# Optimization experiments

Hardware: AMD Instinct MI355X
Metric: run time of the kernel (lower is better)

The kernel has to match this reference:

```python
import jax, jax.numpy as jnp
import numpy as np

B = 20000       # batch (labeled) nodes
N1 = 80000      # first-order neighbor nodes
E = 800000      # edges in the sampled subgraph over B+N1 nodes
C_IN = 256
C_OUT = 256
NUM_D = 32
NB = C_IN // NUM_D   # 8 branches
NUM_M = 4096
NUM_N = 200000  # total graph nodes (c_indices buffer length)


def setup_inputs() -> dict:
    key = jax.random.key(0)
    ks = jax.random.split(key, 12)
    x = jax.random.normal(ks[0], (B, C_IN), dtype=jnp.float32)
    edge_index = jax.random.randint(ks[1], (2, E), 0, B + N1, dtype=jnp.int32)
    edge_weight = jax.random.uniform(ks[2], (E,), dtype=jnp.float32)
    c_indices = jax.random.randint(ks[3], (NB, NUM_N), 0, NUM_M, dtype=jnp.int32)
    first_order_idx = jax.random.randint(ks[4], (N1,), 0, NUM_N, dtype=jnp.int32)
    codebook = jax.random.normal(ks[5], (NB, NUM_M, 2 * NUM_D), dtype=jnp.float32)
    s = 1.0 / np.sqrt(C_IN)
    W_conv = jax.random.normal(ks[6], (C_IN, C_IN), dtype=jnp.float32) * s
    b_conv = jnp.zeros((C_IN,), dtype=jnp.float32)
    W_t = jax.random.normal(ks[7], (C_IN, C_OUT), dtype=jnp.float32) * s
    b_t = jnp.zeros((C_OUT,), dtype=jnp.float32)
    W_skip = jax.random.normal(ks[8], (C_IN, C_OUT), dtype=jnp.float32) * s
    b_skip = jnp.zeros((C_OUT,), dtype=jnp.float32)
    warm_up_rate = jnp.ones((1,), dtype=jnp.float32)
    return {
        'x': x, 'edge_weight': edge_weight, 'codebook': codebook,
        'W_conv': W_conv, 'b_conv': b_conv, 'W_t': W_t, 'b_t': b_t,
        'W_skip': W_skip, 'b_skip': b_skip, 'warm_up_rate': warm_up_rate,
        'c_indices': c_indices, 'first_order_idx': first_order_idx,
        'edge_index': edge_index,
    }


def reference(x, edge_weight, codebook, W_conv, b_conv, W_t, b_t,
              W_skip, b_skip, warm_up_rate, c_indices, first_order_idx,
              edge_index):
    nb = codebook.shape[0]
    D = codebook.shape[2] // 2
    n_total = x.shape[0] + first_order_idx.shape[0]

    # per-branch VQ codebook gather for first-order neighbors: [nb, N1, 2D]
    c_idx = c_indices[:, first_order_idx]                       # [nb, N1]
    cb = codebook[jnp.arange(nb)[:, None], c_idx]               # [nb, N1, 2D]
    # concat branches along feature dim -> [N1, nb*D]
    x_first_order = cb[:, :, :D].transpose(1, 0, 2).reshape(-1, nb * D)
    grad_first_order = cb[:, :, D:].transpose(1, 0, 2).reshape(-1, nb * D)

    # x_input = [batch rows; quantized neighbor rows]
    x_input = jnp.concatenate([x, x_first_order], axis=0)       # [B+N1, C]

    # GCN conv (normalize=False): aggregate (x@W) over weighted edges + bias
    xw = x_input @ W_conv                                       # [B+N1, C]
    msg = xw[edge_index[0]] * edge_weight[:, None]              # [E, C]
    x_output = jax.ops.segment_sum(msg, edge_index[1],
                                   num_segments=n_total) + b_conv

    # info_backward term (gradient pathway through quantized neighbors)
    info_backward = jnp.sum(x_output[x.shape[0]:] * grad_first_order) \
        * warm_up_rate[0]

    # output transform + skip connection on batch rows only
    out = x_output[:x.shape[0]] @ W_t + b_t + (x @ W_skip + b_skip)
    return out, info_backward
```

## Files before the change

### kernel.cpp

```cpp
#include <hip/hip_runtime.h>

#define B_NODES 20000
#define N1_NODES 80000
#define NTOT 100000
#define E_EDGES 800000
#define CIN 256
#define COUT 256
#define NUM_D 32
#define NB 8
#define NUM_M 4096
#define NUM_N 200000
#define NPART 2048
#define CAP 40
#define NXCVT 313
#define NZERO 100
#define NG1 3126
#define EPB 256
#define NG2 626

typedef __attribute__((ext_vector_type(8))) short short8;
typedef __attribute__((ext_vector_type(8))) unsigned short ushort8;
typedef __attribute__((ext_vector_type(4))) float f32x4;
typedef __attribute__((ext_vector_type(4))) int i32x4;

__device__ inline unsigned short f2bf(float f) {
    unsigned int u = __float_as_uint(f);
    u += 0x7FFFu + ((u >> 16) & 1u);
    return (unsigned short)(u >> 16);
}
__device__ inline float bf2f(unsigned short u) {
    return __uint_as_float((unsigned int)u << 16);
}

__device__ inline short8 pack2(float4 a, float4 b) {
    short8 r;
    r[0] = (short)f2bf(a.x); r[1] = (short)f2bf(a.y);
    r[2] = (short)f2bf(a.z); r[3] = (short)f2bf(a.w);
    r[4] = (short)f2bf(b.x); r[5] = (short)f2bf(b.y);
    r[6] = (short)f2bf(b.z); r[7] = (short)f2bf(b.w);
    return r;
}

__global__ __launch_bounds__(256) void prepw_kernel(
    const float* __restrict__ Wc, const float* __restrict__ Wt,
    const float* __restrict__ Ws, short* __restrict__ WcT,
    short* __restrict__ WoT, const float* __restrict__ x,
    unsigned short* __restrict__ xb, int* __restrict__ cnt)
{
    __shared__ float Ls[64][65];
    if (blockIdx.x < 48) {
        const int z   = blockIdx.x >> 4;
        const int rem = blockIdx.x & 15;
        const int kx  = rem & 3, ny = rem >> 2;
        const float* src = (z == 0) ? Wc : ((z == 1) ? Wt : Ws);
        short* dst = (z == 0) ? WcT : WoT;
        const int dstStride = (z == 0) ? 256 : 512;
        const int colOff = (z == 2) ? 256 : 0;

        const int k0 = kx * 64, n0 = ny * 64;
        const int tid = threadIdx.x;
        #pragma unroll
        for (int lp = 0; lp < 16; ++lp) {
            int idx = tid + lp * 256;
            int rr = idx >> 6, cc = idx & 63;
            Ls[rr][cc] = src[(size_t)(k0 + rr) * 256 + n0 + cc];
        }
        __syncthreads();
        #pragma unroll
        for (int lp = 0; lp < 16; ++lp) {
            int idx = tid + lp * 256;
            int rr = idx >> 6, cc = idx & 63;
            dst[(size_t)(n0 + rr) * dstStride + colOff + k0 + cc] =
                (short)f2bf(Ls[cc][rr]);
        }
    } else if (blockIdx.x < 48 + NXCVT) {
        const int base = (blockIdx.x - 48) * 256 + threadIdx.x;
        const int total8 = B_NODES * CIN / 8;
        for (int g = base; g < total8; g += NXCVT * 256) {
            const float4* src = (const float4*)(x + (size_t)g * 8);
            *(short8*)(xb + (size_t)g * 8) = pack2(src[0], src[1]);
        }
    } else {
        const int base = (blockIdx.x - 48 - NXCVT) * 256 + threadIdx.x;
        const int total4 = (NTOT + NPART) / 4;
        i32x4 z = {0, 0, 0, 0};
        for (int g = base; g < total4; g += NZERO * 256)
            ((i32x4*)cnt)[g] = z;
    }
}

__global__ __launch_bounds__(256) void gemm1_scat_kernel(
    const unsigned short* __restrict__ xb, const int* __restrict__ fo,
    const int* __restrict__ cind, const float* __restrict__ cb,
    const short* __restrict__ WcT, unsigned short* __restrict__ xwb,
    const int* __restrict__ ei, const float* __restrict__ ew,
    int* __restrict__ cnt, int2* __restrict__ esw)
{
    __shared__ short As[2][64 * 40];
    __shared__ short Bs[2][128 * 40];

    const int tid  = threadIdx.x;
    const int w    = tid >> 6, l = tid & 63;
    const int row0 = (blockIdx.x >> 1) * 64;
    const int colbase = (blockIdx.x & 1) * 128;
    const int r    = tid >> 2, q = tid & 3;
    const int bc_  = tid >> 1, bq = tid & 1;
    const int grow = row0 + r;
    const int g16  = (l >> 4) * 8;

    f32x4 acc[4][2] = {};

    for (int kso = 0; kso < 4; ++kso) {
        #pragma unroll
        for (int h = 0; h < 2; ++h) {
            const int ks = kso * 2 + h;
            const int k0 = ks * 32;
            short8 sv = {0,0,0,0,0,0,0,0};
            if (grow < B_NODES) {
                sv = *(const short8*)(xb + (size_t)grow * CIN + k0 + q * 8);
            } else if (grow < NTOT) {
                int i = grow - B_NODES;
                int cidx = cind[ks * NUM_N + fo[i]];
                const float4* src = (const float4*)(cb +
                    ((size_t)(ks * NUM_M + cidx)) * (2 * NUM_D) + q * 8);
                sv = pack2(src[0], src[1]);
            }
            *(short8*)&As[h][r * 40 + q * 8] = sv;

            const short8* wp = (const short8*)(WcT +
                (size_t)(colbase + bc_) * 256 + k0 + bq * 16);
            short8* bd = (short8*)&Bs[h][bc_ * 40 + bq * 16];
            bd[0] = wp[0]; bd[1] = wp[1];
        }
        __syncthreads();

        #pragma unroll
        for (int h = 0; h < 2; ++h) {
            short8 av[4], bv[2];
            #pragma unroll
            for (int m = 0; m < 4; ++m)
                av[m] = *(const short8*)&As[h][((l & 15) + 16 * m) * 40 + g16];
            #pragma unroll
            for (int n = 0; n < 2; ++n)
                bv[n] = *(const short8*)&Bs[h][((l & 15) + 16 * n + w * 32) * 40 + g16];
            #pragma unroll
            for (int m = 0; m < 4; ++m)
                #pragma unroll
                for (int n = 0; n < 2; ++n)
                    acc[m][n] = __builtin_amdgcn_mfma_f32_16x16x32_bf16(
                        av[m], bv[n], acc[m][n], 0, 0, 0);
        }
        __syncthreads();
    }

    #pragma unroll
    for (int m = 0; m < 4; ++m) {
        int rbase = row0 + 16 * m + (l >> 4) * 4;
        #pragma unroll
        for (int n = 0; n < 2; ++n) {
            int col = colbase + w * 32 + 16 * n + (l & 15);
            #pragma unroll
            for (int j = 0; j < 4; ++j) {
                int rr = rbase + j;
                if (rr < NTOT)
                    xwb[(size_t)rr * COUT + col] = f2bf(acc[m][n][j]);
            }
        }
    }

    int e = blockIdx.x * EPB + tid;
    if (e < E_EDGES) {
        int dst = ei[E_EDGES + e];
        int pos = atomicAdd(&cnt[dst], 1);
        esw[(size_t)dst * CAP + pos] = make_int2(ei[e], __float_as_int(ew[e]));
    }
}

__global__ __launch_bounds__(256) void gather_accum_kernel(
    const unsigned short* __restrict__ xwb, const int2* __restrict__ esw,
    const int* __restrict__ cnt, const float* __restrict__ b_conv,
    const int* __restrict__ fo, const int* __restrict__ cind,
    const float* __restrict__ cb,
    unsigned short* __restrict__ xoutb, float* __restrict__ scalpart)
{
    const int wid  = threadIdx.x >> 6;
    const int lane = threadIdx.x & 63;
    const int node = blockIdx.x * 4 + wid;
    if (node >= NTOT) return;

    const int half = lane >> 5;
    const int l32  = lane & 31;
    const int c0   = l32 * 8;

    float acc[8];
    if (half == 0) {
        float4 b0 = *(const float4*)(b_conv + c0);
        float4 b1 = *(const float4*)(b_conv + c0 + 4);
        acc[0] = b0.x; acc[1] = b0.y; acc[2] = b0.z; acc[3] = b0.w;
        acc[4] = b1.x; acc[5] = b1.y; acc[6] = b1.z; acc[7] = b1.w;
    } else {
        #pragma unroll
        for (int k = 0; k < 8; ++k) acc[k] = 0.0f;
    }

    const int s = node * CAP;
    const int e = s + cnt[node];
    for (int j = s; j < e; j += 8) {
        int2  p[4];
        float w[4];
        #pragma unroll
        for (int t = 0; t < 4; ++t) {
            int idx = j + 2 * t + half;
            bool valid = idx < e;
            p[t] = esw[valid ? idx : s];
            w[t] = valid ? __int_as_float(p[t].y) : 0.0f;
        }
        ushort8 u[4];
        #pragma unroll
        for (int t = 0; t < 4; ++t)
            u[t] = *(const ushort8*)(xwb + (size_t)p[t].x * CIN + c0);
        #pragma unroll
        for (int t = 0; t < 4; ++t) {
            #pragma unroll
            for (int k = 0; k < 8; ++k) acc[k] += bf2f(u[t][k]) * w[t];
        }
    }

    #pragma unroll
    for (int k = 0; k < 8; ++k) acc[k] += __shfl_xor(acc[k], 32, 64);

    if (node < B_NODES) {
        if (half == 0) {
            ushort8 o;
            #pragma unroll
            for (int k = 0; k < 8; ++k) o[k] = f2bf(acc[k]);
            *(ushort8*)(xoutb + (size_t)node * CIN + c0) = o;
        }
    } else {
        float v = 0.0f;
        if (half == 0) {
            int i = node - B_NODES;
            int b = l32 >> 2;
            int d = (l32 & 3) * 8;
            int cidx = cind[b * NUM_N + fo[i]];
            const float* gp = cb + ((size_t)(b * NUM_M + cidx)) * (2 * NUM_D)
                              + NUM_D + d;
            float4 g0 = *(const float4*)gp;
            float4 g1 = *(const float4*)(gp + 4);
            v = acc[0] * g0.x + acc[1] * g0.y + acc[2] * g0.z + acc[3] * g0.w
              + acc[4] * g1.x + acc[5] * g1.y + acc[6] * g1.z + acc[7] * g1.w;
        }
        #pragma unroll
        for (int off = 32; off > 0; off >>= 1) v += __shfl_down(v, off, 64);
        if (lane == 0)
            atomicAdd(&scalpart[node & (NPART - 1)], v);
    }
}

__global__ __launch_bounds__(256) void gemm2_fin_kernel(
    const unsigned short* __restrict__ xoutb, const unsigned short* __restrict__ xb,
    const short* __restrict__ WoT,
    const float* __restrict__ bt, const float* __restrict__ bskip,
    const float* __restrict__ scalpart, const float* __restrict__ wur,
    float* __restrict__ out)
{
    if (blockIdx.x == NG2) {
        __shared__ float wsum[4];
        float v = 0.0f;
        for (int i = threadIdx.x; i < NPART; i += 256) v += scalpart[i];
        #pragma unroll
        for (int off = 32; off > 0; off >>= 1) v += __shfl_down(v, off, 64);
        if ((threadIdx.x & 63) == 0) wsum[threadIdx.x >> 6] = v;
        __syncthreads();
        if (threadIdx.x == 0)
            out[(size_t)B_NODES * COUT] =
                (wsum[0] + wsum[1] + wsum[2] + wsum[3]) * wur[0];
        return;
    }

    __shared__ short As[2][64 * 40];
    __shared__ short Bs[2][128 * 40];
    __shared__ float bsum[128];

    const int tid  = threadIdx.x;
    const int w    = tid >> 6, l = tid & 63;
    const int row0 = (blockIdx.x >> 1) * 64;
    const int colbase = (blockIdx.x & 1) * 128;
    const int r    = tid >> 2, q = tid & 3;
    const int bc_  = tid >> 1, bq = tid & 1;
    const int grow = row0 + r;
    const int g16  = (l >> 4) * 8;

    if (tid < 128) bsum[tid] = bt[colbase + tid] + bskip[colbase + tid];

    f32x4 acc[4][2] = {};

    for (int kso = 0; kso < 8; ++kso) {
        #pragma unroll
        for (int h = 0; h < 2; ++h) {
            const int ks = kso * 2 + h;
            const int k0 = ks * 32;
            short8 sv = {0,0,0,0,0,0,0,0};
            if (grow < B_NODES) {
                const unsigned short* base = (ks < 8)
                    ? (xoutb + (size_t)grow * CIN + k0)
                    : (xb    + (size_t)grow * CIN + (k0 - 256));
                sv = *(const short8*)(base + q * 8);
            }
            *(short8*)&As[h][r * 40 + q * 8] = sv;

            const short8* wp = (const short8*)(WoT +
                (size_t)(colbase + bc_) * 512 + k0 + bq * 16);
            short8* bd = (short8*)&Bs[h][bc_ * 40 + bq * 16];
            bd[0] = wp[0]; bd[1] = wp[1];
        }
        __syncthreads();

        #pragma unroll
        for (int h = 0; h < 2; ++h) {
            short8 av[4], bv[2];
            #pragma unroll
            for (int m = 0; m < 4; ++m)
                av[m] = *(const short8*)&As[h][((l & 15) + 16 * m) * 40 + g16];
            #pragma unroll
            for (int n = 0; n < 2; ++n)
                bv[n] = *(const short8*)&Bs[h][((l & 15) + 16 * n + w * 32) * 40 + g16];
            #pragma unroll
            for (int m = 0; m < 4; ++m)
                #pragma unroll
                for (int n = 0; n < 2; ++n)
                    acc[m][n] = __builtin_amdgcn_mfma_f32_16x16x32_bf16(
                        av[m], bv[n], acc[m][n], 0, 0, 0);
        }
        __syncthreads();
    }

    #pragma unroll
    for (int m = 0; m < 4; ++m) {
        int rbase = row0 + 16 * m + (l >> 4) * 4;
        #pragma unroll
        for (int n = 0; n < 2; ++n) {
            int lcol = w * 32 + 16 * n + (l & 15);
            int col  = colbase + lcol;
            float bc = bsum[lcol];
            #pragma unroll
            for (int j = 0; j < 4; ++j) {
                int rr = rbase + j;
                if (rr < B_NODES)
                    out[(size_t)rr * COUT + col] = acc[m][n][j] + bc;
            }
        }
    }
}

extern "C" void kernel_launch(void* const* d_in, const int* in_sizes, int n_in,
                              void* d_out, int out_size, void* d_ws, size_t ws_size,
                              hipStream_t stream)
{
    const float* x       = (const float*)d_in[0];
    const float* ew      = (const float*)d_in[1];
    const float* cb      = (const float*)d_in[2];
    const float* W_conv  = (const float*)d_in[3];
    const float* b_conv  = (const float*)d_in[4];
    const float* W_t     = (const float*)d_in[5];
    const float* b_t     = (const float*)d_in[6];
    const float* W_skip  = (const float*)d_in[7];
    const float* b_skip  = (const float*)d_in[8];
    const float* wur     = (const float*)d_in[9];
    const int*   cind    = (const int*)d_in[10];
    const int*   fo      = (const int*)d_in[11];
    const int*   ei      = (const int*)d_in[12];

    float* out = (float*)d_out;

    unsigned short* xwb   = (unsigned short*)d_ws;
    unsigned short* xoutb = xwb + (size_t)NTOT * CIN;
    unsigned short* xb    = xoutb + (size_t)B_NODES * CIN;
    short* WcT      = (short*)(xb + (size_t)B_NODES * CIN);
    short* WoT      = WcT + 256 * 256;
    int2*  esw      = (int2*)(WoT + 256 * 512);
    int*   cnt      = (int*)(esw + (size_t)NTOT * CAP);
    float* scalpart = (float*)(cnt + NTOT);

    prepw_kernel<<<48 + NXCVT + NZERO, 256, 0, stream>>>(
        W_conv, W_t, W_skip, WcT, WoT, x, xb, cnt);

    gemm1_scat_kernel<<<NG1, 256, 0, stream>>>(
        xb, fo, cind, cb, WcT, xwb, ei, ew, cnt, esw);

    gather_accum_kernel<<<NTOT / 4, 256, 0, stream>>>(
        xwb, esw, cnt, b_conv, fo, cind, cb, xoutb, scalpart);

    gemm2_fin_kernel<<<NG2 + 1, 256, 0, stream>>>(
        xoutb, xb, WoT, b_t, b_skip, scalpart, wur, out);
}
```

Before: 178.0 us.

## Widen GEMM1 tiles to full 256 columns with 512-thread blocks

The first GEMM now uses 512-thread blocks that each compute a 64x256 output tile, instead of two 256-thread blocks sharing a row tile at 128 columns each. Each codebook gather and the x row load now happen once per row tile rather than twice, and first_order_idx is read once before the K loop. The double-buffered K-step pairs become single 32-wide steps, so there are more barriers per tile. Each block also takes on 512 edges for the scatter.

```diff
diff --git a/kernel.cpp b/kernel.cpp
--- a/kernel.cpp
+++ b/kernel.cpp
@@ -13,12 +13,13 @@
 #define NPART 2048
 #define CAP 40
 #define NXCVT 313
-#define NZERO 100
-#define NG1 3126
-#define EPB 256
+#define NZB 100
+#define NG1 1563
 #define NG2 626
+#define EPB1 512
 
 typedef __attribute__((ext_vector_type(8))) short short8;
+typedef __attribute__((ext_vector_type(4))) short s16x4;
 typedef __attribute__((ext_vector_type(8))) unsigned short ushort8;
 typedef __attribute__((ext_vector_type(4))) float f32x4;
 typedef __attribute__((ext_vector_type(4))) int i32x4;
@@ -38,6 +39,12 @@
     r[2] = (short)f2bf(a.z); r[3] = (short)f2bf(a.w);
     r[4] = (short)f2bf(b.x); r[5] = (short)f2bf(b.y);
     r[6] = (short)f2bf(b.z); r[7] = (short)f2bf(b.w);
+    return r;
+}
+__device__ inline s16x4 pack1(float4 a) {
+    s16x4 r;
+    r[0] = (short)f2bf(a.x); r[1] = (short)f2bf(a.y);
+    r[2] = (short)f2bf(a.z); r[3] = (short)f2bf(a.w);
     return r;
 }
 
@@ -84,72 +91,66 @@
         const int base = (blockIdx.x - 48 - NXCVT) * 256 + threadIdx.x;
         const int total4 = (NTOT + NPART) / 4;
         i32x4 z = {0, 0, 0, 0};
-        for (int g = base; g < total4; g += NZERO * 256)
+        for (int g = base; g < total4; g += NZB * 256)
             ((i32x4*)cnt)[g] = z;
     }
 }
 
-__global__ __launch_bounds__(256) void gemm1_scat_kernel(
+__global__ __launch_bounds__(512) void gemm1_scat_kernel(
     const unsigned short* __restrict__ xb, const int* __restrict__ fo,
     const int* __restrict__ cind, const float* __restrict__ cb,
     const short* __restrict__ WcT, unsigned short* __restrict__ xwb,
     const int* __restrict__ ei, const float* __restrict__ ew,
     int* __restrict__ cnt, int2* __restrict__ esw)
 {
-    __shared__ short As[2][64 * 40];
-    __shared__ short Bs[2][128 * 40];
+    __shared__ short As[64 * 40];
+    __shared__ short Bs[256 * 40];
 
     const int tid  = threadIdx.x;
     const int w    = tid >> 6, l = tid & 63;
-    const int row0 = (blockIdx.x >> 1) * 64;
-    const int colbase = (blockIdx.x & 1) * 128;
-    const int r    = tid >> 2, q = tid & 3;
-    const int bc_  = tid >> 1, bq = tid & 1;
+    const int row0 = blockIdx.x * 64;
+    const int r    = tid >> 3, q = tid & 7;
+    const int bcol = tid >> 1, bq = tid & 1;
     const int grow = row0 + r;
     const int g16  = (l >> 4) * 8;
 
+    const int fi = (grow >= B_NODES && grow < NTOT) ? fo[grow - B_NODES] : 0;
+
     f32x4 acc[4][2] = {};
 
-    for (int kso = 0; kso < 4; ++kso) {
-        #pragma unroll
-        for (int h = 0; h < 2; ++h) {
-            const int ks = kso * 2 + h;
-            const int k0 = ks * 32;
-            short8 sv = {0,0,0,0,0,0,0,0};
-            if (grow < B_NODES) {
-                sv = *(const short8*)(xb + (size_t)grow * CIN + k0 + q * 8);
-            } else if (grow < NTOT) {
-                int i = grow - B_NODES;
-                int cidx = cind[ks * NUM_N + fo[i]];
-                const float4* src = (const float4*)(cb +
-                    ((size_t)(ks * NUM_M + cidx)) * (2 * NUM_D) + q * 8);
-                sv = pack2(src[0], src[1]);
-            }
-            *(short8*)&As[h][r * 40 + q * 8] = sv;
-
-            const short8* wp = (const short8*)(WcT +
-                (size_t)(colbase + bc_) * 256 + k0 + bq * 16);
-            short8* bd = (short8*)&Bs[h][bc_ * 40 + bq * 16];
+    for (int ks = 0; ks < 8; ++ks) {
+        const int k0 = ks * 32;
+        s16x4 sv = {0, 0, 0, 0};
+        if (grow < B_NODES) {
+            sv = *(const s16x4*)(xb + (size_t)grow * CIN + k0 + q * 4);
+        } else if (grow < NTOT) {
+            int cidx = cind[ks * NUM_N + fi];
+            float4 f = *(const float4*)(cb +
+                ((size_t)(ks * NUM_M + cidx)) * (2 * NUM_D) + q * 4);
+            sv = pack1(f);
+        }
+        *(s16x4*)&As[r * 40 + q * 4] = sv;
+
+        {
+            const short8* wp = (const short8*)(WcT + (size_t)bcol * 256 + k0 + bq * 16);
+            short8* bd = (short8*)&Bs[bcol * 40 + bq * 16];
             bd[0] = wp[0]; bd[1] = wp[1];
         }
         __syncthreads();
 
-        #pragma unroll
-        for (int h = 0; h < 2; ++h) {
-            short8 av[4], bv[2];
-            #pragma unroll
-            for (int m = 0; m < 4; ++m)
-                av[m] = *(const short8*)&As[h][((l & 15) + 16 * m) * 40 + g16];
+        short8 av[4], bv[2];
+        #pragma unroll
+        for (int m = 0; m < 4; ++m)
+            av[m] = *(const short8*)&As[((l & 15) + 16 * m) * 40 + g16];
+        #pragma unroll
+        for (int n = 0; n < 2; ++n)
+            bv[n] = *(const short8*)&Bs[((l & 15) + 16 * n + w * 32) * 40 + g16];
+        #pragma unroll
+        for (int m = 0; m < 4; ++m)
             #pragma unroll
             for (int n = 0; n < 2; ++n)
-                bv[n] = *(const short8*)&Bs[h][((l & 15) + 16 * n + w * 32) * 40 + g16];
-            #pragma unroll
-            for (int m = 0; m < 4; ++m)
-                #pragma unroll
-                for (int n = 0; n < 2; ++n)
-                    acc[m][n] = __builtin_amdgcn_mfma_f32_16x16x32_bf16(
-                        av[m], bv[n], acc[m][n], 0, 0, 0);
-        }
+                acc[m][n] = __builtin_amdgcn_mfma_f32_16x16x32_bf16(
+                    av[m], bv[n], acc[m][n], 0, 0, 0);
         __syncthreads();
     }
 
@@ -158,7 +159,7 @@
         int rbase = row0 + 16 * m + (l >> 4) * 4;
         #pragma unroll
         for (int n = 0; n < 2; ++n) {
-            int col = colbase + w * 32 + 16 * n + (l & 15);
+            int col = w * 32 + 16 * n + (l & 15);
             #pragma unroll
             for (int j = 0; j < 4; ++j) {
                 int rr = rbase + j;
@@ -168,7 +169,7 @@
         }
     }
 
-    int e = blockIdx.x * EPB + tid;
+    int e = blockIdx.x * EPB1 + tid;
     if (e < E_EDGES) {
         int dst = ei[E_EDGES + e];
         int pos = atomicAdd(&cnt[dst], 1);
@@ -382,10 +383,10 @@
     int*   cnt      = (int*)(esw + (size_t)NTOT * CAP);
     float* scalpart = (float*)(cnt + NTOT);
 
-    prepw_kernel<<<48 + NXCVT + NZERO, 256, 0, stream>>>(
+    prepw_kernel<<<48 + NXCVT + NZB, 256, 0, stream>>>(
         W_conv, W_t, W_skip, WcT, WoT, x, xb, cnt);
 
-    gemm1_scat_kernel<<<NG1, 256, 0, stream>>>(
+    gemm1_scat_kernel<<<NG1, 512, 0, stream>>>(
         xb, fo, cind, cb, WcT, xwb, ei, ew, cnt, esw);
 
     gather_accum_kernel<<<NTOT / 4, 256, 0, stream>>>(
```

Result: no change. 176.4 us (-0.9%).
